# Kernel tuning notes

Measured on AMD Instinct MI355X. Metric: run time of the kernel, lower is better.

## Reference

```python
import jax, jax.numpy as jnp
import numpy as np

D_MODEL = 1024
NUM_HEADS = 16
HEAD_DIM = D_MODEL // NUM_HEADS


def setup_inputs() -> dict:
    key = jax.random.key(0)
    ks = jax.random.split(key, 5)
    scale = 1.0 / np.sqrt(D_MODEL)
    x = jax.random.normal(ks[0], (2, 2048, D_MODEL), dtype=jnp.float32)
    Wqkv = jax.random.normal(ks[1], (D_MODEL, 3 * D_MODEL), dtype=jnp.float32) * scale
    bqkv = jax.random.normal(ks[2], (3 * D_MODEL,), dtype=jnp.float32) * 0.02
    Wout = jax.random.normal(ks[3], (D_MODEL, D_MODEL), dtype=jnp.float32) * scale
    bout = jax.random.normal(ks[4], (D_MODEL,), dtype=jnp.float32) * 0.02
    return {"x": x, "Wqkv": Wqkv, "bqkv": bqkv, "Wout": Wout, "bout": bout}


def reference(x, Wqkv, bqkv, Wout, bout):
    B, T, D = x.shape
    H, Hd = NUM_HEADS, HEAD_DIM
    # fused QKV projection: [B,T,3D] -> [3,B,H,T,Hd]
    qkv = (x @ Wqkv + bqkv).reshape(B, T, 3, H, Hd).transpose(2, 0, 3, 1, 4)
    q, k, v = qkv[0], qkv[1], qkv[2]
    # scaled dot-product attention with full TxT scores (faithful to source)
    scores = jnp.einsum("bhqd,bhkd->bhqk", q, k) / np.sqrt(Hd).astype(np.float32)
    weights = jax.nn.softmax(scores, axis=-1)
    context = jnp.einsum("bhqk,bhkd->bhqd", weights, v)
    context = context.transpose(0, 2, 1, 3).reshape(B, T, D)
    return context @ Wout + bout
```

## Files before the change

### kernel.cpp

```cpp
#include <hip/hip_runtime.h>
#include <hip/hip_bf16.h>

#define D_MODEL 1024
#define T_SEQ   2048
#define BATCH   2
#define NHEADS  16
#define HDIM    64
#define QKVSZ   (BATCH * NHEADS * T_SEQ * HDIM)

#define SCALE_Q 0.18033688011112042f

typedef __bf16 bf16_t;
typedef bf16_t bf16x8  __attribute__((ext_vector_type(8)));
typedef float  f32x4   __attribute__((ext_vector_type(4)));
typedef float  f32x16  __attribute__((ext_vector_type(16)));
typedef unsigned uint32x4 __attribute__((ext_vector_type(4)));

#if __has_builtin(__builtin_amdgcn_exp2f)
#define EXP2F(x) __builtin_amdgcn_exp2f(x)
#else
#define EXP2F(x) exp2f(x)
#endif

__device__ __forceinline__ unsigned short f2bf(float f) {
    union { float f; unsigned u; } v; v.f = f;
    unsigned u = v.u;
    u += 0x7FFFu + ((u >> 16) & 1u);
    return (unsigned short)(u >> 16);
}

__device__ __forceinline__ unsigned pkbf(float a, float b) {
    unsigned r;
    asm("v_cvt_pk_bf16_f32 %0, %1, %2" : "=v"(r) : "v"(a), "v"(b));
    return r;
}

__device__ __forceinline__ void gload16(const unsigned short* g, unsigned short* l) {
    __builtin_amdgcn_global_load_lds(
        (const __attribute__((address_space(1))) void*)g,
        (__attribute__((address_space(3))) void*)l,
        16, 0, 0);
}

__global__ void cvt_f32_bf16(const float* __restrict__ src,
                             unsigned short* __restrict__ dst, int n4) {
    int i = blockIdx.x * blockDim.x + threadIdx.x;
    if (i < n4) {
        float4 v = reinterpret_cast<const float4*>(src)[i];
        ushort4 o;
        o.x = f2bf(v.x); o.y = f2bf(v.y); o.z = f2bf(v.z); o.w = f2bf(v.w);
        reinterpret_cast<ushort4*>(dst)[i] = o;
    }
}

__global__ __launch_bounds__(256) void cvt_transpose(
    const float* __restrict__ src, unsigned short* __restrict__ dst, int K, int N)
{
    __shared__ unsigned short Ls[64][72];
    const int n0 = blockIdx.x * 64, k0 = blockIdx.y * 64;
    const int tid = threadIdx.x;
    #pragma unroll
    for (int it = 0; it < 4; ++it) {
        const int r = it * 16 + (tid >> 4);
        const int c = (tid & 15) * 4;
        float4 v = *reinterpret_cast<const float4*>(src + (size_t)(k0 + r) * N + n0 + c);
        Ls[c + 0][r] = f2bf(v.x); Ls[c + 1][r] = f2bf(v.y);
        Ls[c + 2][r] = f2bf(v.z); Ls[c + 3][r] = f2bf(v.w);
    }
    __syncthreads();
    #pragma unroll
    for (int it = 0; it < 2; ++it) {
        const int rn = it * 32 + (tid >> 3);
        const int ck = (tid & 7) * 8;
        *reinterpret_cast<uint4*>(dst + (size_t)(n0 + rn) * K + k0 + ck) =
            *reinterpret_cast<const uint4*>(&Ls[rn][ck]);
    }
}

__global__ __launch_bounds__(256) void transpose_v(
    const unsigned short* __restrict__ v, unsigned short* __restrict__ vt)
{
    __shared__ unsigned short Ls[64][72];
    const int t0 = blockIdx.x * 64;
    const size_t base = ((size_t)(blockIdx.z * NHEADS + blockIdx.y)) * T_SEQ * HDIM;
    const int tid = threadIdx.x;
    const int r  = tid >> 2;
    const int c0 = (tid & 3) * 16;
    unsigned short tmp[16];
    *reinterpret_cast<uint4*>(&tmp[0]) =
        *reinterpret_cast<const uint4*>(v + base + (size_t)(t0 + r) * HDIM + c0);
    *reinterpret_cast<uint4*>(&tmp[8]) =
        *reinterpret_cast<const uint4*>(v + base + (size_t)(t0 + r) * HDIM + c0 + 8);
    #pragma unroll
    for (int i = 0; i < 16; ++i) Ls[c0 + i][r] = tmp[i];
    __syncthreads();
    const int rn = tid >> 2;
    const int ck = (tid & 3) * 16;
    *reinterpret_cast<uint4*>(vt + base + (size_t)rn * T_SEQ + t0 + ck) =
        *reinterpret_cast<const uint4*>(&Ls[rn][ck]);
    *reinterpret_cast<uint4*>(vt + base + (size_t)rn * T_SEQ + t0 + ck + 8) =
        *reinterpret_cast<const uint4*>(&Ls[rn][ck + 8]);
}

template<int MODE>
__global__ __launch_bounds__(256) void gemm128(
    const unsigned short* __restrict__ A,
    const unsigned short* __restrict__ BT,
    const float* __restrict__ bias,
    unsigned short* __restrict__ qkv,
    float* __restrict__ outf,
    int M, int N, int K)
{
    __shared__ unsigned short As[2][128 * 32];
    __shared__ unsigned short Bs[2][128 * 32];
    const int tid = threadIdx.x, wv = tid >> 6, lane = tid & 63;
    const int wr = wv >> 1, wc = wv & 1;
    const int m0 = blockIdx.y * 128, n0 = blockIdx.x * 128;

    const int srow0 = 32 * wv + (lane >> 2);
    const int skc0  = (lane & 3) ^ ((srow0 >> 1) & 3);
    const int srow1 = srow0 + 16;
    const int skc1  = (lane & 3) ^ ((srow1 >> 1) & 3);

    #define GSTAGE(k0v, bf)                                                     \
        {                                                                       \
            gload16(A  + (size_t)(m0 + srow0) * K + (k0v) + skc0 * 8,           \
                    &As[bf][(32 * wv) * 32]);                                   \
            gload16(BT + (size_t)(n0 + srow0) * K + (k0v) + skc0 * 8,           \
                    &Bs[bf][(32 * wv) * 32]);                                   \
            gload16(A  + (size_t)(m0 + srow1) * K + (k0v) + skc1 * 8,           \
                    &As[bf][(32 * wv + 16) * 32]);                              \
            gload16(BT + (size_t)(n0 + srow1) * K + (k0v) + skc1 * 8,           \
                    &Bs[bf][(32 * wv + 16) * 32]);                              \
        }

    f32x4 acc[4][4] = {};

    GSTAGE(0, 0);
    __syncthreads();

    const int nk = K >> 5;
    for (int k = 0; k < nk; ++k) {
        const int cur = k & 1;
        if (k + 1 < nk) GSTAGE((k + 1) << 5, cur ^ 1);

        bf16x8 af[4], bfr[4];
        #pragma unroll
        for (int m = 0; m < 4; ++m) {
            const int row = 64 * wr + 16 * m + (lane & 15);
            const int s   = (lane >> 4) ^ ((row >> 1) & 3);
            af[m] = *reinterpret_cast<const bf16x8*>(&As[cur][row * 32 + s * 8]);
        }
        #pragma unroll
        for (int n = 0; n < 4; ++n) {
            const int row = 64 * wc + 16 * n + (lane & 15);
            const int s   = (lane >> 4) ^ ((row >> 1) & 3);
            bfr[n] = *reinterpret_cast<const bf16x8*>(&Bs[cur][row * 32 + s * 8]);
        }
        #pragma unroll
        for (int m = 0; m < 4; ++m)
            #pragma unroll
            for (int n = 0; n < 4; ++n)
                acc[m][n] = __builtin_amdgcn_mfma_f32_16x16x32_bf16(af[m], bfr[n], acc[m][n], 0, 0, 0);
        __syncthreads();
    }
    #undef GSTAGE

    const int rb = m0 + 64 * wr + ((lane >> 4) << 2);
    const int cb = n0 + 64 * wc + (lane & 15);
    #pragma unroll
    for (int n = 0; n < 4; ++n) {
        const int c = cb + 16 * n;
        const float bc = bias[c];
        #pragma unroll
        for (int m = 0; m < 4; ++m) {
            #pragma unroll
            for (int jr = 0; jr < 4; ++jr) {
                const int r = rb + 16 * m + jr;
                float val = acc[m][n][jr] + bc;
                if (MODE == 0) {
                    const int which = c >> 10;
                    const int rem = c & 1023;
                    const int h = rem >> 6, hd = rem & 63;
                    const int b = r >> 11, t = r & 2047;
                    if (which == 0) val *= SCALE_Q;
                    qkv[(size_t)which * QKVSZ + ((((size_t)b * NHEADS + h) * T_SEQ + t) << 6) + hd] = f2bf(val);
                } else {
                    outf[(size_t)r * N + c] = val;
                }
            }
        }
    }
}

__global__ __launch_bounds__(256) void attn32(
    const unsigned short* __restrict__ qb,
    const unsigned short* __restrict__ kb,
    const unsigned short* __restrict__ vtb,
    unsigned short* __restrict__ ctx)
{
    __shared__ unsigned short Ks[2][64 * 64];
    __shared__ unsigned short Vt[2][64 * 64];

    const int tid = threadIdx.x, wv = tid >> 6, lane = tid & 63;
    const int ql = lane & 31;
    const bool ishi = lane >= 32;
    const int hi = ishi ? 1 : 0;
    const int qt = blockIdx.x, h = blockIdx.y, b = blockIdx.z;

    const size_t base = ((size_t)(b * NHEADS + h)) * T_SEQ * HDIM;
    const unsigned short* Kp  = kb  + base;
    const unsigned short* Vtp = vtb + base;
    const unsigned short* Qp  = qb  + base + ((size_t)qt * 128 + wv * 32 + ql) * HDIM;

    bf16x8 qf0 = *reinterpret_cast<const bf16x8*>(Qp + 0  + hi * 8);
    bf16x8 qf1 = *reinterpret_cast<const bf16x8*>(Qp + 16 + hi * 8);
    bf16x8 qf2 = *reinterpret_cast<const bf16x8*>(Qp + 32 + hi * 8);
    bf16x8 qf3 = *reinterpret_cast<const bf16x8*>(Qp + 48 + hi * 8);

    const int srow = lane >> 3;
    const int ssl  = lane & 7;
    #define STAGE(kt, bf)                                                         \
        {                                                                         \
            _Pragma("unroll")                                                     \
            for (int ihalf = 0; ihalf < 2; ++ihalf) {                             \
                const int g   = wv * 2 + ihalf;                                   \
                const int row = 8 * g + srow;                                     \
                const int sl  = ssl ^ (row & 7) ^ ((row >> 3) & 3);               \
                gload16(Kp  + (size_t)((kt) * 64 + row) * HDIM + sl * 8,          \
                        &Ks[bf][g * 512]);                                        \
                gload16(Vtp + (size_t)row * T_SEQ + (kt) * 64 + sl * 8,           \
                        &Vt[bf][g * 512]);                                        \
            }                                                                     \
        }

    STAGE(0, 0);
    __syncthreads();

    const int kx = (ql & 7) ^ ((ql >> 3) & 3);

    float m = -1e30f, l = 0.f;
    f32x16 o0 = {}, o1 = {};

    for (int kt = 0; kt < T_SEQ / 64; ++kt) {
        const int cur = kt & 1;
        if (kt + 1 < T_SEQ / 64) STAGE(kt + 1, cur ^ 1);

        f32x16 s0 = {}, s1 = {};
        #pragma unroll
        for (int c = 0; c < 4; ++c) {
            const int sw = (2 * c + hi) ^ kx;
            const bf16x8 k0 = *reinterpret_cast<const bf16x8*>(&Ks[cur][(ql)      * 64 + sw * 8]);
            const bf16x8 k1 = *reinterpret_cast<const bf16x8*>(&Ks[cur][(32 + ql) * 64 + sw * 8]);
            const bf16x8 qc = (c == 0) ? qf0 : (c == 1) ? qf1 : (c == 2) ? qf2 : qf3;
            s0 = __builtin_amdgcn_mfma_f32_32x32x16_bf16(k0, qc, s0, 0, 0, 0);
            s1 = __builtin_amdgcn_mfma_f32_32x32x16_bf16(k1, qc, s1, 0, 0, 0);
        }

        float mx = s0[0];
        #pragma unroll
        for (int r = 1; r < 16; ++r) mx = fmaxf(mx, s0[r]);
        #pragma unroll
        for (int r = 0; r < 16; ++r) mx = fmaxf(mx, s1[r]);
        mx = fmaxf(mx, __shfl_xor(mx, 32));

        if (__any(mx > m + 8.0f)) {
            const float mn = fmaxf(m, mx);
            const float sc = EXP2F(m - mn);
            l *= sc; m = mn;
            #pragma unroll
            for (int r = 0; r < 16; ++r) { o0[r] *= sc; o1[r] *= sc; }
        }

        float rs = 0.f;
        #pragma unroll
        for (int r = 0; r < 16; ++r) { const float p = EXP2F(s0[r] - m); s0[r] = p; rs += p; }
        #pragma unroll
        for (int r = 0; r < 16; ++r) { const float p = EXP2F(s1[r] - m); s1[r] = p; rs += p; }
        l += rs + __shfl_xor(rs, 32);

        #pragma unroll
        for (int kc = 0; kc < 4; ++kc) {
            unsigned u0, u1, v0, v1;
            if (kc == 0) {
                u0 = pkbf(s0[0], s0[1]);  u1 = pkbf(s0[2], s0[3]);
                v0 = pkbf(s0[4], s0[5]);  v1 = pkbf(s0[6], s0[7]);
            } else if (kc == 1) {
                u0 = pkbf(s0[8], s0[9]);  u1 = pkbf(s0[10], s0[11]);
                v0 = pkbf(s0[12], s0[13]); v1 = pkbf(s0[14], s0[15]);
            } else if (kc == 2) {
                u0 = pkbf(s1[0], s1[1]);  u1 = pkbf(s1[2], s1[3]);
                v0 = pkbf(s1[4], s1[5]);  v1 = pkbf(s1[6], s1[7]);
            } else {
                u0 = pkbf(s1[8], s1[9]);  u1 = pkbf(s1[10], s1[11]);
                v0 = pkbf(s1[12], s1[13]); v1 = pkbf(s1[14], s1[15]);
            }
            const unsigned t0 = ishi ? u0 : v0;
            const unsigned t1 = ishi ? u1 : v1;
            const unsigned r0 = __shfl_xor((int)t0, 32);
            const unsigned r1 = __shfl_xor((int)t1, 32);
            uint32x4 fw;
            fw.x = ishi ? r0 : u0;
            fw.y = ishi ? r1 : u1;
            fw.z = ishi ? v0 : r0;
            fw.w = ishi ? v1 : r1;
            const bf16x8 pa = __builtin_bit_cast(bf16x8, fw);

            const int sw = (2 * kc + hi) ^ kx;
            const bf16x8 vva = *reinterpret_cast<const bf16x8*>(&Vt[cur][(ql)      * 64 + sw * 8]);
            const bf16x8 vvb = *reinterpret_cast<const bf16x8*>(&Vt[cur][(32 + ql) * 64 + sw * 8]);
            o0 = __builtin_amdgcn_mfma_f32_32x32x16_bf16(vva, pa, o0, 0, 0, 0);
            o1 = __builtin_amdgcn_mfma_f32_32x32x16_bf16(vvb, pa, o1, 0, 0, 0);
        }

        __syncthreads();
    }

    const float invl = 1.0f / l;
    const int t = qt * 128 + wv * 32 + ql;
    unsigned short* crow = ctx + ((size_t)b * T_SEQ + t) * D_MODEL + h * HDIM;
    #pragma unroll
    for (int r4 = 0; r4 < 4; ++r4) {
        const int d0 = 8 * r4 + 4 * hi;
        ushort4 w;
        w.x = f2bf(o0[4 * r4 + 0] * invl);
        w.y = f2bf(o0[4 * r4 + 1] * invl);
        w.z = f2bf(o0[4 * r4 + 2] * invl);
        w.w = f2bf(o0[4 * r4 + 3] * invl);
        *reinterpret_cast<ushort4*>(crow + d0) = w;
        w.x = f2bf(o1[4 * r4 + 0] * invl);
        w.y = f2bf(o1[4 * r4 + 1] * invl);
        w.z = f2bf(o1[4 * r4 + 2] * invl);
        w.w = f2bf(o1[4 * r4 + 3] * invl);
        *reinterpret_cast<ushort4*>(crow + 32 + d0) = w;
    }
}

extern "C" void kernel_launch(void* const* d_in, const int* in_sizes, int n_in,
                              void* d_out, int out_size, void* d_ws, size_t ws_size,
                              hipStream_t stream) {
    const float* x    = (const float*)d_in[0];
    const float* Wqkv = (const float*)d_in[1];
    const float* bqkv = (const float*)d_in[2];
    const float* Wout = (const float*)d_in[3];
    const float* bout = (const float*)d_in[4];
    float* out = (float*)d_out;

    char* ws = (char*)d_ws;
    unsigned short* xb    = (unsigned short*)(ws);
    unsigned short* wqkvT = (unsigned short*)(ws + 8388608);
    unsigned short* woutT = (unsigned short*)(ws + 14680064);
    unsigned short* qkv   = (unsigned short*)(ws + 16777216);
    unsigned short* ctx   = (unsigned short*)(ws + 41943040);

    int n4 = (BATCH * T_SEQ * D_MODEL) / 4;
    cvt_f32_bf16<<<(n4 + 255) / 256, 256, 0, stream>>>(x, xb, n4);

    dim3 gt1(3 * D_MODEL / 64, D_MODEL / 64);
    cvt_transpose<<<gt1, 256, 0, stream>>>(Wqkv, wqkvT, D_MODEL, 3 * D_MODEL);
    dim3 gt2(D_MODEL / 64, D_MODEL / 64);
    cvt_transpose<<<gt2, 256, 0, stream>>>(Wout, woutT, D_MODEL, D_MODEL);

    dim3 g1(3 * D_MODEL / 128, (BATCH * T_SEQ) / 128);
    gemm128<0><<<g1, 256, 0, stream>>>(xb, wqkvT, bqkv, qkv, nullptr,
                                       BATCH * T_SEQ, 3 * D_MODEL, D_MODEL);

    dim3 gtv(T_SEQ / 64, NHEADS, BATCH);
    transpose_v<<<gtv, 256, 0, stream>>>(qkv + (size_t)2 * QKVSZ, xb);

    dim3 g2(T_SEQ / 128, NHEADS, BATCH);
    attn32<<<g2, 256, 0, stream>>>(qkv,
                                   qkv + (size_t)QKVSZ,
                                   xb,
                                   ctx);

    dim3 g3(D_MODEL / 128, (BATCH * T_SEQ) / 128);
    gemm128<1><<<g3, 256, 0, stream>>>(ctx, woutT, bout, nullptr, out,
                                       BATCH * T_SEQ, D_MODEL, D_MODEL);
}
```

Before: 139.4 us.

## Split attention KV range across two wave groups and merge partial softmax states

The attention kernel now runs 512 threads per block: two groups of four waves each process half of the key sequence for the same 128 queries. At the end they merge their partial outputs and (m, l) softmax statistics through LDS. The V transpose kernel permutes keys within each 16-wide group so the P fragment can be fed to MFMA without cross-lane shuffles. Max and sum reductions are restructured into parallel trees. This doubles parallelism per block and removes per-iteration shuffles, at the cost of double the LDS footprint, an extra merge step and lower block occupancy.

Result: faster. 132.3 us (-5.1%).

```diff
diff --git a/kernel.cpp b/kernel.cpp
--- a/kernel.cpp
+++ b/kernel.cpp
@@ -96,10 +96,18 @@
     __syncthreads();
     const int rn = tid >> 2;
     const int ck = (tid & 3) * 16;
+    const int a  = ck >> 4;
+    const int kb = 32 * (a >> 1) + 16 * (a & 1);
+    unsigned short buf[16];
+    #pragma unroll
+    for (int i = 0; i < 16; ++i) {
+        const int key = kb + 4 * (i >> 3) + 8 * ((i & 7) >> 2) + (i & 3);
+        buf[i] = Ls[rn][key];
+    }
     *reinterpret_cast<uint4*>(vt + base + (size_t)rn * T_SEQ + t0 + ck) =
-        *reinterpret_cast<const uint4*>(&Ls[rn][ck]);
+        *reinterpret_cast<const uint4*>(&buf[0]);
     *reinterpret_cast<uint4*>(vt + base + (size_t)rn * T_SEQ + t0 + ck + 8) =
-        *reinterpret_cast<const uint4*>(&Ls[rn][ck + 8]);
+        *reinterpret_cast<const uint4*>(&buf[8]);
 }
 
 template<int MODE>
@@ -193,44 +201,45 @@
     }
 }
 
-__global__ __launch_bounds__(256) void attn32(
+__global__ __launch_bounds__(512) void attn32(
     const unsigned short* __restrict__ qb,
     const unsigned short* __restrict__ kb,
     const unsigned short* __restrict__ vtb,
     unsigned short* __restrict__ ctx)
 {
-    __shared__ unsigned short Ks[2][64 * 64];
-    __shared__ unsigned short Vt[2][64 * 64];
-
-    const int tid = threadIdx.x, wv = tid >> 6, lane = tid & 63;
+    __shared__ unsigned short Ks[2][2][64 * 64];
+    __shared__ unsigned short Vt[2][2][64 * 64];
+
+    const int tid = threadIdx.x;
+    const int wv = tid >> 6, lane = tid & 63;
+    const int wg = wv >> 2, wl = wv & 3;
     const int ql = lane & 31;
-    const bool ishi = lane >= 32;
-    const int hi = ishi ? 1 : 0;
+    const int hi = lane >> 5;
     const int qt = blockIdx.x, h = blockIdx.y, b = blockIdx.z;
 
     const size_t base = ((size_t)(b * NHEADS + h)) * T_SEQ * HDIM;
     const unsigned short* Kp  = kb  + base;
     const unsigned short* Vtp = vtb + base;
-    const unsigned short* Qp  = qb  + base + ((size_t)qt * 128 + wv * 32 + ql) * HDIM;
-
-    bf16x8 qf0 = *reinterpret_cast<const bf16x8*>(Qp + 0  + hi * 8);
-    bf16x8 qf1 = *reinterpret_cast<const bf16x8*>(Qp + 16 + hi * 8);
-    bf16x8 qf2 = *reinterpret_cast<const bf16x8*>(Qp + 32 + hi * 8);
-    bf16x8 qf3 = *reinterpret_cast<const bf16x8*>(Qp + 48 + hi * 8);
+    const unsigned short* Qp  = qb  + base + ((size_t)qt * 128 + wl * 32 + ql) * HDIM;
+
+    const bf16x8 qf0 = *reinterpret_cast<const bf16x8*>(Qp + 0  + hi * 8);
+    const bf16x8 qf1 = *reinterpret_cast<const bf16x8*>(Qp + 16 + hi * 8);
+    const bf16x8 qf2 = *reinterpret_cast<const bf16x8*>(Qp + 32 + hi * 8);
+    const bf16x8 qf3 = *reinterpret_cast<const bf16x8*>(Qp + 48 + hi * 8);
 
     const int srow = lane >> 3;
     const int ssl  = lane & 7;
-    #define STAGE(kt, bf)                                                         \
+    #define STAGE(i, bf)                                                          \
         {                                                                         \
             _Pragma("unroll")                                                     \
             for (int ihalf = 0; ihalf < 2; ++ihalf) {                             \
-                const int g   = wv * 2 + ihalf;                                   \
-                const int row = 8 * g + srow;                                     \
+                const int g2  = wl * 2 + ihalf;                                   \
+                const int row = 8 * g2 + srow;                                    \
                 const int sl  = ssl ^ (row & 7) ^ ((row >> 3) & 3);               \
-                gload16(Kp  + (size_t)((kt) * 64 + row) * HDIM + sl * 8,          \
-                        &Ks[bf][g * 512]);                                        \
-                gload16(Vtp + (size_t)row * T_SEQ + (kt) * 64 + sl * 8,           \
-                        &Vt[bf][g * 512]);                                        \
+                gload16(Kp  + (size_t)((wg * 16 + (i)) * 64 + row) * HDIM + sl * 8, \
+                        &Ks[wg][bf][g2 * 512]);                                   \
+                gload16(Vtp + (size_t)row * T_SEQ + (wg * 16 + (i)) * 64 + sl * 8, \
+                        &Vt[wg][bf][g2 * 512]);                                   \
             }                                                                     \
         }
 
@@ -242,26 +251,30 @@
     float m = -1e30f, l = 0.f;
     f32x16 o0 = {}, o1 = {};
 
-    for (int kt = 0; kt < T_SEQ / 64; ++kt) {
-        const int cur = kt & 1;
-        if (kt + 1 < T_SEQ / 64) STAGE(kt + 1, cur ^ 1);
+    for (int i = 0; i < 16; ++i) {
+        const int cur = i & 1;
+        if (i + 1 < 16) STAGE(i + 1, cur ^ 1);
 
         f32x16 s0 = {}, s1 = {};
         #pragma unroll
         for (int c = 0; c < 4; ++c) {
             const int sw = (2 * c + hi) ^ kx;
-            const bf16x8 k0 = *reinterpret_cast<const bf16x8*>(&Ks[cur][(ql)      * 64 + sw * 8]);
-            const bf16x8 k1 = *reinterpret_cast<const bf16x8*>(&Ks[cur][(32 + ql) * 64 + sw * 8]);
+            const bf16x8 k0 = *reinterpret_cast<const bf16x8*>(&Ks[wg][cur][(ql)      * 64 + sw * 8]);
+            const bf16x8 k1 = *reinterpret_cast<const bf16x8*>(&Ks[wg][cur][(32 + ql) * 64 + sw * 8]);
             const bf16x8 qc = (c == 0) ? qf0 : (c == 1) ? qf1 : (c == 2) ? qf2 : qf3;
             s0 = __builtin_amdgcn_mfma_f32_32x32x16_bf16(k0, qc, s0, 0, 0, 0);
             s1 = __builtin_amdgcn_mfma_f32_32x32x16_bf16(k1, qc, s1, 0, 0, 0);
         }
 
-        float mx = s0[0];
-        #pragma unroll
-        for (int r = 1; r < 16; ++r) mx = fmaxf(mx, s0[r]);
-        #pragma unroll
-        for (int r = 0; r < 16; ++r) mx = fmaxf(mx, s1[r]);
+        float a0 = fmaxf(s0[0], s0[4]), a1 = fmaxf(s0[1], s0[5]);
+        float a2 = fmaxf(s0[2], s0[6]), a3 = fmaxf(s0[3], s0[7]);
+        a0 = fmaxf(a0, fmaxf(s0[8],  s0[12]));  a1 = fmaxf(a1, fmaxf(s0[9],  s0[13]));
+        a2 = fmaxf(a2, fmaxf(s0[10], s0[14])); a3 = fmaxf(a3, fmaxf(s0[11], s0[15]));
+        a0 = fmaxf(a0, fmaxf(s1[0], s1[4]));   a1 = fmaxf(a1, fmaxf(s1[1], s1[5]));
+        a2 = fmaxf(a2, fmaxf(s1[2], s1[6]));   a3 = fmaxf(a3, fmaxf(s1[3], s1[7]));
+        a0 = fmaxf(a0, fmaxf(s1[8],  s1[12])); a1 = fmaxf(a1, fmaxf(s1[9],  s1[13]));
+        a2 = fmaxf(a2, fmaxf(s1[10], s1[14])); a3 = fmaxf(a3, fmaxf(s1[11], s1[15]));
+        float mx = fmaxf(fmaxf(a0, a1), fmaxf(a2, a3));
         mx = fmaxf(mx, __shfl_xor(mx, 32));
 
         if (__any(mx > m + 8.0f)) {
@@ -272,67 +285,86 @@
             for (int r = 0; r < 16; ++r) { o0[r] *= sc; o1[r] *= sc; }
         }
 
-        float rs = 0.f;
-        #pragma unroll
-        for (int r = 0; r < 16; ++r) { const float p = EXP2F(s0[r] - m); s0[r] = p; rs += p; }
-        #pragma unroll
-        for (int r = 0; r < 16; ++r) { const float p = EXP2F(s1[r] - m); s1[r] = p; rs += p; }
+        #pragma unroll
+        for (int r = 0; r < 16; ++r) s0[r] = EXP2F(s0[r] - m);
+        #pragma unroll
+        for (int r = 0; r < 16; ++r) s1[r] = EXP2F(s1[r] - m);
+        float b0 = 0.f, b1 = 0.f, b2 = 0.f, b3 = 0.f;
+        #pragma unroll
+        for (int r = 0; r < 16; r += 4) {
+            b0 += s0[r]; b1 += s0[r + 1]; b2 += s0[r + 2]; b3 += s0[r + 3];
+            b0 += s1[r]; b1 += s1[r + 1]; b2 += s1[r + 2]; b3 += s1[r + 3];
+        }
+        float rs = (b0 + b1) + (b2 + b3);
         l += rs + __shfl_xor(rs, 32);
 
         #pragma unroll
         for (int kc = 0; kc < 4; ++kc) {
-            unsigned u0, u1, v0, v1;
+            uint32x4 fw;
             if (kc == 0) {
-                u0 = pkbf(s0[0], s0[1]);  u1 = pkbf(s0[2], s0[3]);
-                v0 = pkbf(s0[4], s0[5]);  v1 = pkbf(s0[6], s0[7]);
+                fw.x = pkbf(s0[0], s0[1]);   fw.y = pkbf(s0[2], s0[3]);
+                fw.z = pkbf(s0[4], s0[5]);   fw.w = pkbf(s0[6], s0[7]);
             } else if (kc == 1) {
-                u0 = pkbf(s0[8], s0[9]);  u1 = pkbf(s0[10], s0[11]);
-                v0 = pkbf(s0[12], s0[13]); v1 = pkbf(s0[14], s0[15]);
+                fw.x = pkbf(s0[8], s0[9]);   fw.y = pkbf(s0[10], s0[11]);
+                fw.z = pkbf(s0[12], s0[13]); fw.w = pkbf(s0[14], s0[15]);
             } else if (kc == 2) {
-                u0 = pkbf(s1[0], s1[1]);  u1 = pkbf(s1[2], s1[3]);
-                v0 = pkbf(s1[4], s1[5]);  v1 = pkbf(s1[6], s1[7]);
+                fw.x = pkbf(s1[0], s1[1]);   fw.y = pkbf(s1[2], s1[3]);
+                fw.z = pkbf(s1[4], s1[5]);   fw.w = pkbf(s1[6], s1[7]);
             } else {
-                u0 = pkbf(s1[8], s1[9]);  u1 = pkbf(s1[10], s1[11]);
-                v0 = pkbf(s1[12], s1[13]); v1 = pkbf(s1[14], s1[15]);
+                fw.x = pkbf(s1[8], s1[9]);   fw.y = pkbf(s1[10], s1[11]);
+                fw.z = pkbf(s1[12], s1[13]); fw.w = pkbf(s1[14], s1[15]);
             }
-            const unsigned t0 = ishi ? u0 : v0;
-            const unsigned t1 = ishi ? u1 : v1;
-            const unsigned r0 = __shfl_xor((int)t0, 32);
-            const unsigned r1 = __shfl_xor((int)t1, 32);
-            uint32x4 fw;
-            fw.x = ishi ? r0 : u0;
-            fw.y = ishi ? r1 : u1;
-            fw.z = ishi ? v0 : r0;
-            fw.w = ishi ? v1 : r1;
             const bf16x8 pa = __builtin_bit_cast(bf16x8, fw);
-
             const int sw = (2 * kc + hi) ^ kx;
-            const bf16x8 vva = *reinterpret_cast<const bf16x8*>(&Vt[cur][(ql)      * 64 + sw * 8]);
-            const bf16x8 vvb = *reinterpret_cast<const bf16x8*>(&Vt[cur][(32 + ql) * 64 + sw * 8]);
+            const bf16x8 vva = *reinterpret_cast<const bf16x8*>(&Vt[wg][cur][(ql)      * 64 + sw * 8]);
+            const bf16x8 vvb = *reinterpret_cast<const bf16x8*>(&Vt[wg][cur][(32 + ql) * 64 + sw * 8]);
             o0 = __builtin_amdgcn_mfma_f32_32x32x16_bf16(vva, pa, o0, 0, 0, 0);
             o1 = __builtin_amdgcn_mfma_f32_32x32x16_bf16(vvb, pa, o1, 0, 0, 0);
         }
 
         __syncthreads();
     }
-
-    const float invl = 1.0f / l;
-    const int t = qt * 128 + wv * 32 + ql;
-    unsigned short* crow = ctx + ((size_t)b * T_SEQ + t) * D_MODEL + h * HDIM;
-    #pragma unroll
-    for (int r4 = 0; r4 < 4; ++r4) {
-        const int d0 = 8 * r4 + 4 * hi;
-        ushort4 w;
-        w.x = f2bf(o0[4 * r4 + 0] * invl);
-        w.y = f2bf(o0[4 * r4 + 1] * invl);
-        w.z = f2bf(o0[4 * r4 + 2] * invl);
-        w.w = f2bf(o0[4 * r4 + 3] * invl);
-        *reinterpret_cast<ushort4*>(crow + d0) = w;
-        w.x = f2bf(o1[4 * r4 + 0] * invl);
-        w.y = f2bf(o1[4 * r4 + 1] * invl);
-        w.z = f2bf(o1[4 * r4 + 2] * invl);
-        w.w = f2bf(o1[4 * r4 + 3] * invl);
-        *reinterpret_cast<ushort4*>(crow + 32 + d0) = w;
+    #undef STAGE
+
+    float* xo0  = (float*)&Ks[0][0][0];
+    float* xo1m = (float*)&Vt[0][0][0];
+    const int idx = wl * 64 + lane;
+    if (wg == 1) {
+        float* pa0 = xo0 + idx * 17;
+        float* pb0 = xo1m + idx * 19;
+        #pragma unroll
+        for (int r = 0; r < 16; ++r) pa0[r] = o0[r];
+        #pragma unroll
+        for (int r = 0; r < 16; ++r) pb0[r] = o1[r];
+        pb0[16] = m; pb0[17] = l;
+    }
+    __syncthreads();
+    if (wg == 0) {
+        const float* pa0 = xo0 + idx * 17;
+        const float* pb0 = xo1m + idx * 19;
+        const float m2 = pb0[16], l2 = pb0[17];
+        const float mn = fmaxf(m, m2);
+        const float ca = EXP2F(m - mn), cb = EXP2F(m2 - mn);
+        const float invl = 1.0f / (l * ca + l2 * cb);
+        const float fa = ca * invl, fb = cb * invl;
+
+        const int t = qt * 128 + wl * 32 + ql;
+        unsigned short* crow = ctx + ((size_t)b * T_SEQ + t) * D_MODEL + h * HDIM;
+        #pragma unroll
+        for (int r4 = 0; r4 < 4; ++r4) {
+            const int d0 = 8 * r4 + 4 * hi;
+            ushort4 w;
+            w.x = f2bf(o0[4 * r4 + 0] * fa + pa0[4 * r4 + 0] * fb);
+            w.y = f2bf(o0[4 * r4 + 1] * fa + pa0[4 * r4 + 1] * fb);
+            w.z = f2bf(o0[4 * r4 + 2] * fa + pa0[4 * r4 + 2] * fb);
+            w.w = f2bf(o0[4 * r4 + 3] * fa + pa0[4 * r4 + 3] * fb);
+            *reinterpret_cast<ushort4*>(crow + d0) = w;
+            w.x = f2bf(o1[4 * r4 + 0] * fa + pb0[4 * r4 + 0] * fb);
+            w.y = f2bf(o1[4 * r4 + 1] * fa + pb0[4 * r4 + 1] * fb);
+            w.z = f2bf(o1[4 * r4 + 2] * fa + pb0[4 * r4 + 2] * fb);
+            w.w = f2bf(o1[4 * r4 + 3] * fa + pb0[4 * r4 + 3] * fb);
+            *reinterpret_cast<ushort4*>(crow + 32 + d0) = w;
+        }
     }
 }
 
@@ -369,7 +401,7 @@
     transpose_v<<<gtv, 256, 0, stream>>>(qkv + (size_t)2 * QKVSZ, xb);
 
     dim3 g2(T_SEQ / 128, NHEADS, BATCH);
-    attn32<<<g2, 256, 0, stream>>>(qkv,
+    attn32<<<g2, 512, 0, stream>>>(qkv,
                                    qkv + (size_t)QKVSZ,
                                    xb,
                                    ctx);
```
